# Performance work log

Measured on AMD Instinct MI355X. Metric: run time of the kernel, lower is better.

Reference implementation:

```python
import jax, jax.numpy as jnp
import numpy as np

B, V, H, K = 2048, 4096, 1024, 5

def setup_inputs() -> dict:
    key = jax.random.key(0)
    k1, k2, k3, k4, k5, k6, k7 = jax.random.split(key, 7)
    return {
        "visible_example": (jax.random.uniform(k1, (B, V)) > 0.5).astype(jnp.float32),
        "b_v": jax.random.normal(k2, (V,), jnp.float32) * 0.1,
        "b_h": jax.random.normal(k3, (H,), jnp.float32) * 0.1,
        "W": jax.random.normal(k4, (V, H), jnp.float32) * 0.02,
        "u_h0": jax.random.uniform(k5, (B, H), jnp.float32),
        "u_v": jax.random.uniform(k6, (K // 2 + 1, B, V), jnp.float32),
        "u_h": jax.random.uniform(k7, (K // 2, B, H), jnp.float32),
    }

def reference(visible_example, b_v, b_h, W, u_h0, u_v, u_h):
    # score(v,h) = -energy = v.b_v + h.b_h + (v @ W) * h summed
    def score(v, h):
        return v @ b_v + h @ b_h + jnp.einsum('bv,vh,bh->b', v, W, h)  # [B]

    def bernoulli(p, u):
        # samples are detached in the original (requires_grad_(False))
        return jax.lax.stop_gradient((p > u).astype(jnp.float32))

    # positive phase: sample h | data
    h = bernoulli(jax.nn.sigmoid(b_h + visible_example @ W), u_h0)  # [B,H]
    log_prob_positive = score(visible_example, h)

    # K-step alternating Gibbs chain: v, h, v, h, v  (statically unrolled)
    v = visible_example
    vi = hi = 0
    for k in range(K):
        if k % 2 == 0:
            v = bernoulli(jax.nn.sigmoid(b_v + h @ W.T), u_v[vi]); vi += 1
        else:
            h = bernoulli(jax.nn.sigmoid(b_h + v @ W), u_h[hi]); hi += 1

    log_prob_negative = score(v, h)
    return log_prob_positive - log_prob_negative  # [B]
```

## Files before the change

kernel.cpp:

```cpp
#include <hip/hip_runtime.h>
#include <math.h>

#define B_DIM 2048
#define V_DIM 4096
#define H_DIM 1024

#define BM 64
#define BN 64
#define BK 16
#define KC 384
#define LDS_STRIDE 68

enum { ACC_NONE = 0, ACC_PREACT = 1, ACC_BIAS = 2 };

__global__ __launch_bounds__(256) void gemm_h_kernel(
    const float* __restrict__ A,
    const float* __restrict__ W,
    const float* __restrict__ bh,
    const float* __restrict__ U,
    float* __restrict__ Hout,
    double* __restrict__ acc,
    const int mode)
{
    __shared__ float As[2][BK][LDS_STRIDE];
    __shared__ float Bs[2][BK][LDS_STRIDE];

    const int bn = blockIdx.x * BN;
    const int bm = blockIdx.y * BM;
    const int t  = threadIdx.x;
    const int tx = t & 15;
    const int ty = t >> 4;

    const int ar  = t >> 2;
    const int ac4 = t & 3;
    const int br  = t >> 4;
    const int bc4 = t & 15;

    float tot[4][4];
    float part[4][4];
#pragma unroll
    for (int i = 0; i < 4; i++)
#pragma unroll
        for (int j = 0; j < 4; j++) { tot[i][j] = 0.0f; part[i][j] = 0.0f; }

    const float* Aptr = A + (size_t)(bm + ar) * V_DIM + ac4 * 4;
    const float* Wptr = W + (size_t)bn + bc4 * 4;

    float4 av = *(const float4*)(Aptr + 0);
    float4 wv = *(const float4*)(Wptr + (size_t)br * H_DIM);
    As[0][ac4 * 4 + 0][ar] = av.x;
    As[0][ac4 * 4 + 1][ar] = av.y;
    As[0][ac4 * 4 + 2][ar] = av.z;
    As[0][ac4 * 4 + 3][ar] = av.w;
    *(float4*)(&Bs[0][br][bc4 * 4]) = wv;

    const int T = V_DIM / BK;
    int cur = 0;
    for (int it = 0; it < T; ++it) {
        __syncthreads();
        if (it + 1 < T) {
            const int k0 = (it + 1) * BK;
            av = *(const float4*)(Aptr + k0);
            wv = *(const float4*)(Wptr + (size_t)(k0 + br) * H_DIM);
        }
#pragma unroll
        for (int k = 0; k < BK; k++) {
            float4 a4 = *(const float4*)(&As[cur][k][ty * 4]);
            float4 b4 = *(const float4*)(&Bs[cur][k][tx * 4]);
            float aa[4] = {a4.x, a4.y, a4.z, a4.w};
            float bb[4] = {b4.x, b4.y, b4.z, b4.w};
#pragma unroll
            for (int i = 0; i < 4; i++)
#pragma unroll
                for (int j = 0; j < 4; j++)
                    part[i][j] = fmaf(aa[i], bb[j], part[i][j]);
        }
        if (it + 1 < T) {
            As[cur ^ 1][ac4 * 4 + 0][ar] = av.x;
            As[cur ^ 1][ac4 * 4 + 1][ar] = av.y;
            As[cur ^ 1][ac4 * 4 + 2][ar] = av.z;
            As[cur ^ 1][ac4 * 4 + 3][ar] = av.w;
            *(float4*)(&Bs[cur ^ 1][br][bc4 * 4]) = wv;
        }
        cur ^= 1;
        if ((((it + 1) * BK) % KC) == 0) {
#pragma unroll
            for (int i = 0; i < 4; i++)
#pragma unroll
                for (int j = 0; j < 4; j++) { tot[i][j] += part[i][j]; part[i][j] = 0.0f; }
        }
    }
    if ((V_DIM % KC) != 0) {
#pragma unroll
        for (int i = 0; i < 4; i++)
#pragma unroll
            for (int j = 0; j < 4; j++) tot[i][j] += part[i][j];
    }

    double rowacc[4] = {0.0, 0.0, 0.0, 0.0};
#pragma unroll
    for (int i = 0; i < 4; i++) {
        const int row = bm + ty * 4 + i;
#pragma unroll
        for (int j = 0; j < 4; j++) {
            const int col = bn + tx * 4 + j;
            float bias = bh[col];
            float pre = bias + tot[i][j];
            float p = 1.0f / (1.0f + expf(-pre));
            float u = U[(size_t)row * H_DIM + col];
            float hv = (p > u) ? 1.0f : 0.0f;
            Hout[(size_t)row * H_DIM + col] = hv;
            if (mode == ACC_PREACT) rowacc[i] += (double)hv * (double)pre;
            else if (mode == ACC_BIAS) rowacc[i] += (double)hv * (double)bias;
        }
    }
    if (mode != ACC_NONE) {
#pragma unroll
        for (int off = 8; off >= 1; off >>= 1)
#pragma unroll
            for (int i = 0; i < 4; i++)
                rowacc[i] += __shfl_xor(rowacc[i], off, 16);
        if (tx == 0) {
#pragma unroll
            for (int i = 0; i < 4; i++)
                atomicAdd(&acc[bm + ty * 4 + i], rowacc[i]);
        }
    }
}

__global__ __launch_bounds__(256) void gemm_v_kernel(
    const float* __restrict__ A,
    const float* __restrict__ W,
    const float* __restrict__ bv,
    const float* __restrict__ U,
    float* __restrict__ Vout,
    double* __restrict__ acc,
    const int mode)
{
    __shared__ float As[2][BK][LDS_STRIDE];
    __shared__ float Bs[2][BK][LDS_STRIDE];

    const int bn = blockIdx.x * BN;
    const int bm = blockIdx.y * BM;
    const int t  = threadIdx.x;
    const int tx = t & 15;
    const int ty = t >> 4;

    const int ar  = t >> 2;
    const int ac4 = t & 3;

    float tot[4][4];
    float part[4][4];
#pragma unroll
    for (int i = 0; i < 4; i++)
#pragma unroll
        for (int j = 0; j < 4; j++) { tot[i][j] = 0.0f; part[i][j] = 0.0f; }

    const float* Aptr = A + (size_t)(bm + ar) * H_DIM + ac4 * 4;
    const float* Wrow = W + (size_t)(bn + ar) * H_DIM + ac4 * 4;

    float4 av = *(const float4*)(Aptr + 0);
    float4 wv = *(const float4*)(Wrow + 0);
    As[0][ac4 * 4 + 0][ar] = av.x;
    As[0][ac4 * 4 + 1][ar] = av.y;
    As[0][ac4 * 4 + 2][ar] = av.z;
    As[0][ac4 * 4 + 3][ar] = av.w;
    Bs[0][ac4 * 4 + 0][ar] = wv.x;
    Bs[0][ac4 * 4 + 1][ar] = wv.y;
    Bs[0][ac4 * 4 + 2][ar] = wv.z;
    Bs[0][ac4 * 4 + 3][ar] = wv.w;

    const int T = H_DIM / BK;
    int cur = 0;
    for (int it = 0; it < T; ++it) {
        __syncthreads();
        if (it + 1 < T) {
            const int k0 = (it + 1) * BK;
            av = *(const float4*)(Aptr + k0);
            wv = *(const float4*)(Wrow + k0);
        }
#pragma unroll
        for (int k = 0; k < BK; k++) {
            float4 a4 = *(const float4*)(&As[cur][k][ty * 4]);
            float4 b4 = *(const float4*)(&Bs[cur][k][tx * 4]);
            float aa[4] = {a4.x, a4.y, a4.z, a4.w};
            float bb[4] = {b4.x, b4.y, b4.z, b4.w};
#pragma unroll
            for (int i = 0; i < 4; i++)
#pragma unroll
                for (int j = 0; j < 4; j++)
                    part[i][j] = fmaf(aa[i], bb[j], part[i][j]);
        }
        if (it + 1 < T) {
            As[cur ^ 1][ac4 * 4 + 0][ar] = av.x;
            As[cur ^ 1][ac4 * 4 + 1][ar] = av.y;
            As[cur ^ 1][ac4 * 4 + 2][ar] = av.z;
            As[cur ^ 1][ac4 * 4 + 3][ar] = av.w;
            Bs[cur ^ 1][ac4 * 4 + 0][ar] = wv.x;
            Bs[cur ^ 1][ac4 * 4 + 1][ar] = wv.y;
            Bs[cur ^ 1][ac4 * 4 + 2][ar] = wv.z;
            Bs[cur ^ 1][ac4 * 4 + 3][ar] = wv.w;
        }
        cur ^= 1;
        if ((((it + 1) * BK) % KC) == 0) {
#pragma unroll
            for (int i = 0; i < 4; i++)
#pragma unroll
                for (int j = 0; j < 4; j++) { tot[i][j] += part[i][j]; part[i][j] = 0.0f; }
        }
    }
    if ((H_DIM % KC) != 0) {
#pragma unroll
        for (int i = 0; i < 4; i++)
#pragma unroll
            for (int j = 0; j < 4; j++) tot[i][j] += part[i][j];
    }

    double rowacc[4] = {0.0, 0.0, 0.0, 0.0};
#pragma unroll
    for (int i = 0; i < 4; i++) {
        const int row = bm + ty * 4 + i;
#pragma unroll
        for (int j = 0; j < 4; j++) {
            const int col = bn + tx * 4 + j;
            float pre = bv[col] + tot[i][j];
            float p = 1.0f / (1.0f + expf(-pre));
            float u = U[(size_t)row * V_DIM + col];
            float vv = (p > u) ? 1.0f : 0.0f;
            Vout[(size_t)row * V_DIM + col] = vv;
            if (mode == ACC_PREACT) rowacc[i] += (double)vv * (double)pre;
        }
    }
    if (mode != ACC_NONE) {
#pragma unroll
        for (int off = 8; off >= 1; off >>= 1)
#pragma unroll
            for (int i = 0; i < 4; i++)
                rowacc[i] += __shfl_xor(rowacc[i], off, 16);
        if (tx == 0) {
#pragma unroll
            for (int i = 0; i < 4; i++)
                atomicAdd(&acc[bm + ty * 4 + i], rowacc[i]);
        }
    }
}

__global__ __launch_bounds__(256) void rowdot_kernel(
    const float* __restrict__ X, const float* __restrict__ w,
    double* __restrict__ out, const int N)
{
    const int b = blockIdx.x;
    const float* row = X + (size_t)b * N;
    double s = 0.0;
    for (int i = threadIdx.x; i < N / 4; i += blockDim.x) {
        float4 x = ((const float4*)row)[i];
        float4 ww = ((const float4*)w)[i];
        s = fma((double)x.x, (double)ww.x, s);
        s = fma((double)x.y, (double)ww.y, s);
        s = fma((double)x.z, (double)ww.z, s);
        s = fma((double)x.w, (double)ww.w, s);
    }
#pragma unroll
    for (int off = 32; off >= 1; off >>= 1) s += __shfl_xor(s, off, 64);
    __shared__ double red[4];
    if ((threadIdx.x & 63) == 0) red[threadIdx.x >> 6] = s;
    __syncthreads();
    if (threadIdx.x == 0) out[b] = red[0] + red[1] + red[2] + red[3];
}

__global__ void finalize_kernel(const double* __restrict__ vb,
                                const double* __restrict__ accpos,
                                const double* __restrict__ acchb,
                                const double* __restrict__ accneg,
                                float* __restrict__ out)
{
    int b = blockIdx.x * blockDim.x + threadIdx.x;
    if (b < B_DIM) out[b] = (float)(vb[b] + accpos[b] - acchb[b] - accneg[b]);
}

extern "C" void kernel_launch(void* const* d_in, const int* in_sizes, int n_in,
                              void* d_out, int out_size, void* d_ws, size_t ws_size,
                              hipStream_t stream) {
    (void)in_sizes; (void)n_in; (void)out_size; (void)ws_size;
    const float* visible = (const float*)d_in[0];
    const float* b_v     = (const float*)d_in[1];
    const float* b_h     = (const float*)d_in[2];
    const float* W       = (const float*)d_in[3];
    const float* u_h0    = (const float*)d_in[4];
    const float* u_v     = (const float*)d_in[5];
    const float* u_h     = (const float*)d_in[6];
    float* out = (float*)d_out;

    float* v_buf   = (float*)d_ws;
    float* h_buf   = v_buf + (size_t)B_DIM * V_DIM;
    double* acc_pos = (double*)(h_buf + (size_t)B_DIM * H_DIM);
    double* acc_hb  = acc_pos + B_DIM;
    double* acc_neg = acc_hb + B_DIM;
    double* vb      = acc_neg + B_DIM;

    hipMemsetAsync(acc_pos, 0, 3 * B_DIM * sizeof(double), stream);

    dim3 blk(256);
    dim3 gh(H_DIM / BN, B_DIM / BM);
    dim3 gv(V_DIM / BN, B_DIM / BM);

    rowdot_kernel<<<B_DIM, blk, 0, stream>>>(visible, b_v, vb, V_DIM);

    const size_t UV = (size_t)B_DIM * V_DIM;
    const size_t UH = (size_t)B_DIM * H_DIM;

    gemm_h_kernel<<<gh, blk, 0, stream>>>(visible, W, b_h, u_h0, h_buf, acc_pos, ACC_PREACT);
    gemm_v_kernel<<<gv, blk, 0, stream>>>(h_buf, W, b_v, u_v + 0 * UV, v_buf, nullptr, ACC_NONE);
    gemm_h_kernel<<<gh, blk, 0, stream>>>(v_buf, W, b_h, u_h + 0 * UH, h_buf, nullptr, ACC_NONE);
    gemm_v_kernel<<<gv, blk, 0, stream>>>(h_buf, W, b_v, u_v + 1 * UV, v_buf, nullptr, ACC_NONE);
    gemm_h_kernel<<<gh, blk, 0, stream>>>(v_buf, W, b_h, u_h + 1 * UH, h_buf, acc_hb, ACC_BIAS);
    gemm_v_kernel<<<gv, blk, 0, stream>>>(h_buf, W, b_v, u_v + 2 * UV, v_buf, acc_neg, ACC_PREACT);

    finalize_kernel<<<(B_DIM + 255) / 256, blk, 0, stream>>>(vb, acc_pos, acc_hb, acc_neg, out);
}
```

Baseline: 1.475 ms.

## Split GEMMs into 128x128 split-K panels with separate combine/sample kernels

After: 2.538 ms. +72.1%, slower.

```diff
diff --git a/kernel.cpp b/kernel.cpp
--- a/kernel.cpp
+++ b/kernel.cpp
@@ -4,40 +4,275 @@
 #define B_DIM 2048
 #define V_DIM 4096
 #define H_DIM 1024
+#define KC 384
+
+#define NPANELS_H ((V_DIM + KC - 1) / KC)
+#define NPANELS_V ((H_DIM + KC - 1) / KC)
+
+enum { ACC_NONE = 0, ACC_PREACT = 1, ACC_BIAS = 2 };
+
+#define PBM 128
+#define PBN 128
+#define PBK 16
+#define ASTRIDE 20
+#define BSTRIDE 132
+
+__global__ __launch_bounds__(256, 4) void gemm_h_panel(
+    const float* __restrict__ A,
+    const float* __restrict__ W,
+    float* __restrict__ P)
+{
+    __shared__ float As[PBM][ASTRIDE];
+    __shared__ float Bs[PBK][BSTRIDE];
+
+    const int p    = blockIdx.z;
+    const int k_lo = p * KC;
+    const int k_ext = (k_lo + KC <= V_DIM) ? KC : (V_DIM - k_lo);
+    const int bn = blockIdx.x * PBN;
+    const int bm = blockIdx.y * PBM;
+    const int t  = threadIdx.x;
+    const int tx = t & 15;
+    const int ty = t >> 4;
+
+    const int arow = t >> 1, ak = (t & 1) * 8;
+    const int bk   = t >> 4, bc = (t & 15) * 8;
+
+    float acc[8][8];
+#pragma unroll
+    for (int i = 0; i < 8; i++)
+#pragma unroll
+        for (int j = 0; j < 8; j++) acc[i][j] = 0.0f;
+
+    const float* Abase = A + (size_t)(bm + arow) * V_DIM + k_lo + ak;
+    const float* Wbase = W + (size_t)(k_lo + bk) * H_DIM + bn + bc;
+
+    const int niter = k_ext / PBK;
+    for (int it = 0; it < niter; ++it) {
+        float4 a0 = *(const float4*)(Abase + it * 16);
+        float4 a1 = *(const float4*)(Abase + it * 16 + 4);
+        float4 b0 = *(const float4*)(Wbase + (size_t)it * 16 * H_DIM);
+        float4 b1 = *(const float4*)(Wbase + (size_t)it * 16 * H_DIM + 4);
+        __syncthreads();
+        *(float4*)&As[arow][ak]     = a0;
+        *(float4*)&As[arow][ak + 4] = a1;
+        *(float4*)&Bs[bk][bc]       = b0;
+        *(float4*)&Bs[bk][bc + 4]   = b1;
+        __syncthreads();
+#pragma unroll
+        for (int kg = 0; kg < 4; kg++) {
+            float ag[8][4];
+#pragma unroll
+            for (int i = 0; i < 4; i++) {
+                float4 lo = *(const float4*)&As[ty * 4 + i][kg * 4];
+                float4 hi = *(const float4*)&As[64 + ty * 4 + i][kg * 4];
+                ag[i][0] = lo.x; ag[i][1] = lo.y; ag[i][2] = lo.z; ag[i][3] = lo.w;
+                ag[4 + i][0] = hi.x; ag[4 + i][1] = hi.y; ag[4 + i][2] = hi.z; ag[4 + i][3] = hi.w;
+            }
+#pragma unroll
+            for (int kk = 0; kk < 4; kk++) {
+                float4 bl = *(const float4*)&Bs[kg * 4 + kk][tx * 4];
+                float4 bh2 = *(const float4*)&Bs[kg * 4 + kk][tx * 4 + 64];
+                float bb[8] = {bl.x, bl.y, bl.z, bl.w, bh2.x, bh2.y, bh2.z, bh2.w};
+#pragma unroll
+                for (int ri = 0; ri < 8; ri++) {
+                    float av = ag[ri][kk];
+#pragma unroll
+                    for (int cj = 0; cj < 8; cj++)
+                        acc[ri][cj] = fmaf(av, bb[cj], acc[ri][cj]);
+                }
+            }
+        }
+    }
+
+    float* Pp = P + (size_t)p * B_DIM * H_DIM;
+#pragma unroll
+    for (int ri = 0; ri < 8; ri++) {
+        const int row = bm + ((ri < 4) ? (ty * 4 + ri) : (64 + ty * 4 + ri - 4));
+        float4 q0 = {acc[ri][0], acc[ri][1], acc[ri][2], acc[ri][3]};
+        float4 q1 = {acc[ri][4], acc[ri][5], acc[ri][6], acc[ri][7]};
+        *(float4*)(Pp + (size_t)row * H_DIM + bn + tx * 4)      = q0;
+        *(float4*)(Pp + (size_t)row * H_DIM + bn + tx * 4 + 64) = q1;
+    }
+}
+
+__global__ __launch_bounds__(256, 4) void gemm_v_panel(
+    const float* __restrict__ A,
+    const float* __restrict__ W,
+    float* __restrict__ P)
+{
+    __shared__ float As[PBK][BSTRIDE];
+    __shared__ float Bs[PBN][ASTRIDE];
+
+    const int p    = blockIdx.z;
+    const int k_lo = p * KC;
+    const int k_ext = (k_lo + KC <= H_DIM) ? KC : (H_DIM - k_lo);
+    const int bn = blockIdx.x * PBN;
+    const int bm = blockIdx.y * PBM;
+    const int t  = threadIdx.x;
+    const int tx = t & 15;
+    const int ty = t >> 4;
+
+    const int arow = t >> 1, ak = (t & 1) * 8;
+    const int bcol = t >> 1, bkq = (t & 1) * 8;
+
+    float acc[8][8];
+#pragma unroll
+    for (int i = 0; i < 8; i++)
+#pragma unroll
+        for (int j = 0; j < 8; j++) acc[i][j] = 0.0f;
+
+    const float* Abase = A + (size_t)(bm + arow) * H_DIM + k_lo + ak;
+    const float* Wbase = W + (size_t)(bn + bcol) * H_DIM + k_lo + bkq;
+
+    const int niter = k_ext / PBK;
+    for (int it = 0; it < niter; ++it) {
+        float4 a0 = *(const float4*)(Abase + it * 16);
+        float4 a1 = *(const float4*)(Abase + it * 16 + 4);
+        float4 b0 = *(const float4*)(Wbase + it * 16);
+        float4 b1 = *(const float4*)(Wbase + it * 16 + 4);
+        __syncthreads();
+        As[ak + 0][arow] = a0.x; As[ak + 1][arow] = a0.y;
+        As[ak + 2][arow] = a0.z; As[ak + 3][arow] = a0.w;
+        As[ak + 4][arow] = a1.x; As[ak + 5][arow] = a1.y;
+        As[ak + 6][arow] = a1.z; As[ak + 7][arow] = a1.w;
+        *(float4*)&Bs[bcol][bkq]     = b0;
+        *(float4*)&Bs[bcol][bkq + 4] = b1;
+        __syncthreads();
+#pragma unroll
+        for (int kg = 0; kg < 4; kg++) {
+            float bg[8][4];
+#pragma unroll
+            for (int i = 0; i < 4; i++) {
+                float4 lo = *(const float4*)&Bs[ty * 4 + i][kg * 4];
+                float4 hi = *(const float4*)&Bs[64 + ty * 4 + i][kg * 4];
+                bg[i][0] = lo.x; bg[i][1] = lo.y; bg[i][2] = lo.z; bg[i][3] = lo.w;
+                bg[4 + i][0] = hi.x; bg[4 + i][1] = hi.y; bg[4 + i][2] = hi.z; bg[4 + i][3] = hi.w;
+            }
+#pragma unroll
+            for (int kk = 0; kk < 4; kk++) {
+                float4 al = *(const float4*)&As[kg * 4 + kk][tx * 4];
+                float4 ah = *(const float4*)&As[kg * 4 + kk][tx * 4 + 64];
+                float aa[8] = {al.x, al.y, al.z, al.w, ah.x, ah.y, ah.z, ah.w};
+#pragma unroll
+                for (int cj = 0; cj < 8; cj++) {
+                    float bv2 = bg[cj][kk];
+#pragma unroll
+                    for (int ri = 0; ri < 8; ri++)
+                        acc[ri][cj] = fmaf(aa[ri], bv2, acc[ri][cj]);
+                }
+            }
+        }
+    }
+
+    float* Pp = P + (size_t)p * B_DIM * V_DIM;
+#pragma unroll
+    for (int ri = 0; ri < 8; ri++) {
+        const int row = bm + ((ri < 4) ? (tx * 4 + ri) : (64 + tx * 4 + ri - 4));
+        float4 q0 = {acc[ri][0], acc[ri][1], acc[ri][2], acc[ri][3]};
+        float4 q1 = {acc[ri][4], acc[ri][5], acc[ri][6], acc[ri][7]};
+        *(float4*)(Pp + (size_t)row * V_DIM + bn + ty * 4)      = q0;
+        *(float4*)(Pp + (size_t)row * V_DIM + bn + ty * 4 + 64) = q1;
+    }
+}
+
+__global__ __launch_bounds__(256) void combine_h(
+    const float* __restrict__ P, const float* __restrict__ bh,
+    const float* __restrict__ U, float* __restrict__ Hout,
+    double* __restrict__ acc, const int mode)
+{
+    const int row = blockIdx.x;
+    const int c = threadIdx.x * 4;
+    float tot[4] = {0.f, 0.f, 0.f, 0.f};
+    for (int p = 0; p < NPANELS_H; p++) {
+        float4 q = *(const float4*)(P + ((size_t)p * B_DIM + row) * H_DIM + c);
+        tot[0] += q.x; tot[1] += q.y; tot[2] += q.z; tot[3] += q.w;
+    }
+    float4 bias = *(const float4*)(bh + c);
+    float4 u4 = *(const float4*)(U + (size_t)row * H_DIM + c);
+    float bb[4] = {bias.x, bias.y, bias.z, bias.w};
+    float uu[4] = {u4.x, u4.y, u4.z, u4.w};
+    float hh[4];
+    double racc = 0.0;
+#pragma unroll
+    for (int j = 0; j < 4; j++) {
+        float pre = bb[j] + tot[j];
+        float pp = 1.0f / (1.0f + expf(-pre));
+        hh[j] = (pp > uu[j]) ? 1.0f : 0.0f;
+        if (mode == ACC_PREACT) racc += (double)hh[j] * (double)pre;
+        else if (mode == ACC_BIAS) racc += (double)hh[j] * (double)bb[j];
+    }
+    float4 hv = {hh[0], hh[1], hh[2], hh[3]};
+    *(float4*)(Hout + (size_t)row * H_DIM + c) = hv;
+
+    if (mode != ACC_NONE) {
+#pragma unroll
+        for (int off = 32; off >= 1; off >>= 1) racc += __shfl_xor(racc, off, 64);
+        __shared__ double red[4];
+        if ((threadIdx.x & 63) == 0) red[threadIdx.x >> 6] = racc;
+        __syncthreads();
+        if (threadIdx.x == 0) acc[row] = ((red[0] + red[1]) + red[2]) + red[3];
+    }
+}
+
+__global__ __launch_bounds__(256) void combine_v(
+    const float* __restrict__ P, const float* __restrict__ bv,
+    const float* __restrict__ U, float* __restrict__ Vout,
+    double* __restrict__ acc, const int mode)
+{
+    const int row = blockIdx.x;
+    double racc = 0.0;
+    for (int jj = 0; jj < 4; jj++) {
+        const int c = (jj * 256 + threadIdx.x) * 4;
+        float tot[4] = {0.f, 0.f, 0.f, 0.f};
+        for (int p = 0; p < NPANELS_V; p++) {
+            float4 q = *(const float4*)(P + ((size_t)p * B_DIM + row) * V_DIM + c);
+            tot[0] += q.x; tot[1] += q.y; tot[2] += q.z; tot[3] += q.w;
+        }
+        float4 bias = *(const float4*)(bv + c);
+        float4 u4 = *(const float4*)(U + (size_t)row * V_DIM + c);
+        float bb[4] = {bias.x, bias.y, bias.z, bias.w};
+        float uu[4] = {u4.x, u4.y, u4.z, u4.w};
+        float vvv[4];
+#pragma unroll
+        for (int j = 0; j < 4; j++) {
+            float pre = bb[j] + tot[j];
+            float pp = 1.0f / (1.0f + expf(-pre));
+            vvv[j] = (pp > uu[j]) ? 1.0f : 0.0f;
+            if (mode == ACC_PREACT) racc += (double)vvv[j] * (double)pre;
+        }
+        float4 vv4 = {vvv[0], vvv[1], vvv[2], vvv[3]};
+        *(float4*)(Vout + (size_t)row * V_DIM + c) = vv4;
+    }
+    if (mode != ACC_NONE) {
+#pragma unroll
+        for (int off = 32; off >= 1; off >>= 1) racc += __shfl_xor(racc, off, 64);
+        __shared__ double red[4];
+        if ((threadIdx.x & 63) == 0) red[threadIdx.x >> 6] = racc;
+        __syncthreads();
+        if (threadIdx.x == 0) acc[row] = ((red[0] + red[1]) + red[2]) + red[3];
+    }
+}
 
 #define BM 64
 #define BN 64
 #define BK 16
-#define KC 384
 #define LDS_STRIDE 68
 
-enum { ACC_NONE = 0, ACC_PREACT = 1, ACC_BIAS = 2 };
-
 __global__ __launch_bounds__(256) void gemm_h_kernel(
-    const float* __restrict__ A,
-    const float* __restrict__ W,
-    const float* __restrict__ bh,
-    const float* __restrict__ U,
-    float* __restrict__ Hout,
-    double* __restrict__ acc,
-    const int mode)
+    const float* __restrict__ A, const float* __restrict__ W,
+    const float* __restrict__ bh, const float* __restrict__ U,
+    float* __restrict__ Hout, double* __restrict__ acc, const int mode)
 {
     __shared__ float As[2][BK][LDS_STRIDE];
     __shared__ float Bs[2][BK][LDS_STRIDE];
-
     const int bn = blockIdx.x * BN;
     const int bm = blockIdx.y * BM;
     const int t  = threadIdx.x;
-    const int tx = t & 15;
-    const int ty = t >> 4;
-
-    const int ar  = t >> 2;
-    const int ac4 = t & 3;
-    const int br  = t >> 4;
-    const int bc4 = t & 15;
-
-    float tot[4][4];
-    float part[4][4];
+    const int tx = t & 15, ty = t >> 4;
+    const int ar = t >> 2, ac4 = t & 3;
+    const int br = t >> 4, bc4 = t & 15;
+
+    float tot[4][4], part[4][4];
 #pragma unroll
     for (int i = 0; i < 4; i++)
 #pragma unroll
@@ -48,10 +283,8 @@
 
     float4 av = *(const float4*)(Aptr + 0);
     float4 wv = *(const float4*)(Wptr + (size_t)br * H_DIM);
-    As[0][ac4 * 4 + 0][ar] = av.x;
-    As[0][ac4 * 4 + 1][ar] = av.y;
-    As[0][ac4 * 4 + 2][ar] = av.z;
-    As[0][ac4 * 4 + 3][ar] = av.w;
+    As[0][ac4 * 4 + 0][ar] = av.x; As[0][ac4 * 4 + 1][ar] = av.y;
+    As[0][ac4 * 4 + 2][ar] = av.z; As[0][ac4 * 4 + 3][ar] = av.w;
     *(float4*)(&Bs[0][br][bc4 * 4]) = wv;
 
     const int T = V_DIM / BK;
@@ -76,10 +309,8 @@
                     part[i][j] = fmaf(aa[i], bb[j], part[i][j]);
         }
         if (it + 1 < T) {
-            As[cur ^ 1][ac4 * 4 + 0][ar] = av.x;
-            As[cur ^ 1][ac4 * 4 + 1][ar] = av.y;
-            As[cur ^ 1][ac4 * 4 + 2][ar] = av.z;
-            As[cur ^ 1][ac4 * 4 + 3][ar] = av.w;
+            As[cur ^ 1][ac4 * 4 + 0][ar] = av.x; As[cur ^ 1][ac4 * 4 + 1][ar] = av.y;
+            As[cur ^ 1][ac4 * 4 + 2][ar] = av.z; As[cur ^ 1][ac4 * 4 + 3][ar] = av.w;
             *(float4*)(&Bs[cur ^ 1][br][bc4 * 4]) = wv;
         }
         cur ^= 1;
@@ -129,28 +360,19 @@
 }
 
 __global__ __launch_bounds__(256) void gemm_v_kernel(
-    const float* __restrict__ A,
-    const float* __restrict__ W,
-    const float* __restrict__ bv,
-    const float* __restrict__ U,
-    float* __restrict__ Vout,
-    double* __restrict__ acc,
-    const int mode)
+    const float* __restrict__ A, const float* __restrict__ W,
+    const float* __restrict__ bv, const float* __restrict__ U,
+    float* __restrict__ Vout, double* __restrict__ acc, const int mode)
 {
     __shared__ float As[2][BK][LDS_STRIDE];
     __shared__ float Bs[2][BK][LDS_STRIDE];
-
     const int bn = blockIdx.x * BN;
     const int bm = blockIdx.y * BM;
     const int t  = threadIdx.x;
-    const int tx = t & 15;
-    const int ty = t >> 4;
-
-    const int ar  = t >> 2;
-    const int ac4 = t & 3;
-
-    float tot[4][4];
-    float part[4][4];
+    const int tx = t & 15, ty = t >> 4;
+    const int ar = t >> 2, ac4 = t & 3;
+
+    float tot[4][4], part[4][4];
 #pragma unroll
     for (int i = 0; i < 4; i++)
 #pragma unroll
@@ -161,14 +383,10 @@
 
     float4 av = *(const float4*)(Aptr + 0);
     float4 wv = *(const float4*)(Wrow + 0);
-    As[0][ac4 * 4 + 0][ar] = av.x;
-    As[0][ac4 * 4 + 1][ar] = av.y;
-    As[0][ac4 * 4 + 2][ar] = av.z;
-    As[0][ac4 * 4 + 3][ar] = av.w;
-    Bs[0][ac4 * 4 + 0][ar] = wv.x;
-    Bs[0][ac4 * 4 + 1][ar] = wv.y;
-    Bs[0][ac4 * 4 + 2][ar] = wv.z;
-    Bs[0][ac4 * 4 + 3][ar] = wv.w;
+    As[0][ac4 * 4 + 0][ar] = av.x; As[0][ac4 * 4 + 1][ar] = av.y;
+    As[0][ac4 * 4 + 2][ar] = av.z; As[0][ac4 * 4 + 3][ar] = av.w;
+    Bs[0][ac4 * 4 + 0][ar] = wv.x; Bs[0][ac4 * 4 + 1][ar] = wv.y;
+    Bs[0][ac4 * 4 + 2][ar] = wv.z; Bs[0][ac4 * 4 + 3][ar] = wv.w;
 
     const int T = H_DIM / BK;
     int cur = 0;
@@ -192,14 +410,10 @@
                     part[i][j] = fmaf(aa[i], bb[j], part[i][j]);
         }
         if (it + 1 < T) {
-            As[cur ^ 1][ac4 * 4 + 0][ar] = av.x;
-            As[cur ^ 1][ac4 * 4 + 1][ar] = av.y;
-            As[cur ^ 1][ac4 * 4 + 2][ar] = av.z;
-            As[cur ^ 1][ac4 * 4 + 3][ar] = av.w;
-            Bs[cur ^ 1][ac4 * 4 + 0][ar] = wv.x;
-            Bs[cur ^ 1][ac4 * 4 + 1][ar] = wv.y;
-            Bs[cur ^ 1][ac4 * 4 + 2][ar] = wv.z;
-            Bs[cur ^ 1][ac4 * 4 + 3][ar] = wv.w;
+            As[cur ^ 1][ac4 * 4 + 0][ar] = av.x; As[cur ^ 1][ac4 * 4 + 1][ar] = av.y;
+            As[cur ^ 1][ac4 * 4 + 2][ar] = av.z; As[cur ^ 1][ac4 * 4 + 3][ar] = av.w;
+            Bs[cur ^ 1][ac4 * 4 + 0][ar] = wv.x; Bs[cur ^ 1][ac4 * 4 + 1][ar] = wv.y;
+            Bs[cur ^ 1][ac4 * 4 + 2][ar] = wv.z; Bs[cur ^ 1][ac4 * 4 + 3][ar] = wv.w;
         }
         cur ^= 1;
         if ((((it + 1) * BK) % KC) == 0) {
@@ -281,7 +495,7 @@
 extern "C" void kernel_launch(void* const* d_in, const int* in_sizes, int n_in,
                               void* d_out, int out_size, void* d_ws, size_t ws_size,
                               hipStream_t stream) {
-    (void)in_sizes; (void)n_in; (void)out_size; (void)ws_size;
+    (void)in_sizes; (void)n_in; (void)out_size;
     const float* visible = (const float*)d_in[0];
     const float* b_v     = (const float*)d_in[1];
     const float* b_h     = (const float*)d_in[2];
@@ -297,24 +511,44 @@
     double* acc_hb  = acc_pos + B_DIM;
     double* acc_neg = acc_hb + B_DIM;
     double* vb      = acc_neg + B_DIM;
-
-    hipMemsetAsync(acc_pos, 0, 3 * B_DIM * sizeof(double), stream);
-
-    dim3 blk(256);
-    dim3 gh(H_DIM / BN, B_DIM / BM);
-    dim3 gv(V_DIM / BN, B_DIM / BM);
-
-    rowdot_kernel<<<B_DIM, blk, 0, stream>>>(visible, b_v, vb, V_DIM);
+    float* P        = (float*)(vb + B_DIM);
 
     const size_t UV = (size_t)B_DIM * V_DIM;
     const size_t UH = (size_t)B_DIM * H_DIM;
-
-    gemm_h_kernel<<<gh, blk, 0, stream>>>(visible, W, b_h, u_h0, h_buf, acc_pos, ACC_PREACT);
-    gemm_v_kernel<<<gv, blk, 0, stream>>>(h_buf, W, b_v, u_v + 0 * UV, v_buf, nullptr, ACC_NONE);
-    gemm_h_kernel<<<gh, blk, 0, stream>>>(v_buf, W, b_h, u_h + 0 * UH, h_buf, nullptr, ACC_NONE);
-    gemm_v_kernel<<<gv, blk, 0, stream>>>(h_buf, W, b_v, u_v + 1 * UV, v_buf, nullptr, ACC_NONE);
-    gemm_h_kernel<<<gh, blk, 0, stream>>>(v_buf, W, b_h, u_h + 1 * UH, h_buf, acc_hb, ACC_BIAS);
-    gemm_v_kernel<<<gv, blk, 0, stream>>>(h_buf, W, b_v, u_v + 2 * UV, v_buf, acc_neg, ACC_PREACT);
+    const size_t pmax = (size_t)NPANELS_H * UH > (size_t)NPANELS_V * UV
+                            ? (size_t)NPANELS_H * UH : (size_t)NPANELS_V * UV;
+    const size_t need = (UV + UH) * 4 + 4 * B_DIM * 8 + pmax * 4;
+
+    dim3 blk(256);
+    rowdot_kernel<<<B_DIM, blk, 0, stream>>>(visible, b_v, vb, V_DIM);
+
+    if (ws_size >= need) {
+        dim3 gph(PBN >= H_DIM ? 1 : H_DIM / PBN, B_DIM / PBM, NPANELS_H);
+        dim3 gpv(V_DIM / PBN, B_DIM / PBM, NPANELS_V);
+
+        gemm_h_panel<<<gph, blk, 0, stream>>>(visible, W, P);
+        combine_h<<<B_DIM, blk, 0, stream>>>(P, b_h, u_h0, h_buf, acc_pos, ACC_PREACT);
+        gemm_v_panel<<<gpv, blk, 0, stream>>>(h_buf, W, P);
+        combine_v<<<B_DIM, blk, 0, stream>>>(P, b_v, u_v + 0 * UV, v_buf, nullptr, ACC_NONE);
+        gemm_h_panel<<<gph, blk, 0, stream>>>(v_buf, W, P);
+        combine_h<<<B_DIM, blk, 0, stream>>>(P, b_h, u_h + 0 * UH, h_buf, nullptr, ACC_NONE);
+        gemm_v_panel<<<gpv, blk, 0, stream>>>(h_buf, W, P);
+        combine_v<<<B_DIM, blk, 0, stream>>>(P, b_v, u_v + 1 * UV, v_buf, nullptr, ACC_NONE);
+        gemm_h_panel<<<gph, blk, 0, stream>>>(v_buf, W, P);
+        combine_h<<<B_DIM, blk, 0, stream>>>(P, b_h, u_h + 1 * UH, h_buf, acc_hb, ACC_BIAS);
+        gemm_v_panel<<<gpv, blk, 0, stream>>>(h_buf, W, P);
+        combine_v<<<B_DIM, blk, 0, stream>>>(P, b_v, u_v + 2 * UV, v_buf, acc_neg, ACC_PREACT);
+    } else {
+        hipMemsetAsync(acc_pos, 0, 3 * B_DIM * sizeof(double), stream);
+        dim3 gh(H_DIM / BN, B_DIM / BM);
+        dim3 gv(V_DIM / BN, B_DIM / BM);
+        gemm_h_kernel<<<gh, blk, 0, stream>>>(visible, W, b_h, u_h0, h_buf, acc_pos, ACC_PREACT);
+        gemm_v_kernel<<<gv, blk, 0, stream>>>(h_buf, W, b_v, u_v + 0 * UV, v_buf, nullptr, ACC_NONE);
+        gemm_h_kernel<<<gh, blk, 0, stream>>>(v_buf, W, b_h, u_h + 0 * UH, h_buf, nullptr, ACC_NONE);
+        gemm_v_kernel<<<gv, blk, 0, stream>>>(h_buf, W, b_v, u_v + 1 * UV, v_buf, nullptr, ACC_NONE);
+        gemm_h_kernel<<<gh, blk, 0, stream>>>(v_buf, W, b_h, u_h + 1 * UH, h_buf, acc_hb, ACC_BIAS);
+        gemm_v_kernel<<<gv, blk, 0, stream>>>(h_buf, W, b_v, u_v + 2 * UV, v_buf, acc_neg, ACC_PREACT);
+    }
 
     finalize_kernel<<<(B_DIM + 255) / 256, blk, 0, stream>>>(vb, acc_pos, acc_hb, acc_neg, out);
 }
```
